# Performance work log

Hardware: AMD Instinct MI355X
Metric: run time of the kernel (lower is better)

Reference implementation:

```python
import jax, jax.numpy as jnp
import numpy as np

B, S, D_IN = 4, 2048, 1024
H, D_HEAD = 16, 64  # num_head, num_out; H*D_HEAD == D_IN here
LN_EPS = 1e-5


def setup_inputs() -> dict:
    key = jax.random.key(0)
    ks = jax.random.split(key, 5)
    scale = 1.0 / np.sqrt(D_IN)
    return {
        "x": jax.random.normal(ks[0], (B, S, D_IN), dtype=jnp.float32),
        "Wq": jax.random.normal(ks[1], (H * D_HEAD, D_IN), dtype=jnp.float32) * scale,
        "Wk": jax.random.normal(ks[2], (H * D_HEAD, D_IN), dtype=jnp.float32) * scale,
        "Wv": jax.random.normal(ks[3], (H * D_HEAD, D_IN), dtype=jnp.float32) * scale,
        "Wr": jax.random.normal(ks[4], (H * D_HEAD, D_IN), dtype=jnp.float32) * scale,
        "gamma": jnp.ones((H * D_HEAD,), dtype=jnp.float32),
        "beta": jnp.zeros((H * D_HEAD,), dtype=jnp.float32),
    }


def reference(x, Wq, Wk, Wv, Wr, gamma, beta):
    b, s, _ = x.shape
    # Linear (no bias), torch weight layout [out, in]; split heads head-major
    q = (x @ Wq.T).reshape(b, s, H, D_HEAD)
    k = (x @ Wk.T).reshape(b, s, H, D_HEAD)
    v = (x @ Wv.T).reshape(b, s, H, D_HEAD)
    # full O(S^2) score matrix, as in the original
    scores = jnp.einsum("bqhd,bkhd->bhqk", q, k) / jnp.sqrt(jnp.float32(D_HEAD))
    weights = jax.nn.softmax(scores, axis=-1)
    attn = jnp.einsum("bhqk,bkhd->bqhd", weights, v).reshape(b, s, H * D_HEAD)
    out = jax.nn.relu(attn + x @ Wr.T)
    # LayerNorm over last dim with affine params
    mu = jnp.mean(out, axis=-1, keepdims=True)
    var = jnp.mean(jnp.square(out - mu), axis=-1, keepdims=True)
    out = (out - mu) * jax.lax.rsqrt(var + LN_EPS) * gamma + beta
    return out
```

## Files before the change

kernel.cpp:

```cpp
#include <hip/hip_runtime.h>
#include <hip/hip_bf16.h>
#include <stdint.h>

constexpr int BB = 4;
constexpr int SS = 2048;
constexpr int DIN = 1024;
constexpr int HH = 16;
constexpr int DH = 64;
constexpr int NOUT = 4096;
constexpr int MROWS = BB * SS;

typedef __attribute__((ext_vector_type(8))) short bf16x8;
typedef __attribute__((ext_vector_type(8))) unsigned short u16x8;
typedef __attribute__((ext_vector_type(4))) unsigned short u16x4;
typedef __attribute__((ext_vector_type(4))) float f32x4;

__device__ __forceinline__ unsigned short f2bf(float f) {
  unsigned int x = __float_as_uint(f);
  unsigned int r = (x + 0x7fffu + ((x >> 16) & 1u)) >> 16;
  return (unsigned short)r;
}
__device__ __forceinline__ float bf2f(unsigned short u) {
  return __uint_as_float(((unsigned int)u) << 16);
}

__device__ __forceinline__ void gload16(const void* g, void* l) {
  typedef __attribute__((address_space(1))) void gvoid;
  typedef __attribute__((address_space(3))) void lvoid;
  __builtin_amdgcn_global_load_lds((gvoid*)(uintptr_t)g, (lvoid*)l, 16, 0, 0);
}

__global__ __launch_bounds__(256) void convert_x(const float* __restrict__ src,
                                                 unsigned short* __restrict__ dst) {
  int i = (blockIdx.x * 256 + threadIdx.x) * 8;
  f32x4 a = *(const f32x4*)(src + i);
  f32x4 b = *(const f32x4*)(src + i + 4);
  u16x8 o;
  o[0] = f2bf(a[0]); o[1] = f2bf(a[1]); o[2] = f2bf(a[2]); o[3] = f2bf(a[3]);
  o[4] = f2bf(b[0]); o[5] = f2bf(b[1]); o[6] = f2bf(b[2]); o[7] = f2bf(b[3]);
  *(u16x8*)(dst + i) = o;
}

__global__ __launch_bounds__(256) void convert_w(const float* __restrict__ Wq,
                                                 const float* __restrict__ Wk,
                                                 const float* __restrict__ Wv,
                                                 const float* __restrict__ Wr,
                                                 unsigned short* __restrict__ dst) {
  int i = (blockIdx.x * 256 + threadIdx.x) * 8;
  int seg = i >> 20;
  const float* src = (seg == 0) ? Wq : (seg == 1) ? Wk : (seg == 2) ? Wv : Wr;
  float scale = (seg == 0) ? 0.125f * 1.44269504088896f : 1.0f;
  int j = i & 1048575;
  f32x4 a = *(const f32x4*)(src + j);
  f32x4 b = *(const f32x4*)(src + j + 4);
  u16x8 o;
  o[0] = f2bf(a[0] * scale); o[1] = f2bf(a[1] * scale);
  o[2] = f2bf(a[2] * scale); o[3] = f2bf(a[3] * scale);
  o[4] = f2bf(b[0] * scale); o[5] = f2bf(b[1] * scale);
  o[6] = f2bf(b[2] * scale); o[7] = f2bf(b[3] * scale);
  *(u16x8*)(dst + i) = o;
}

constexpr int GBM = 128, GBN = 128, GBK = 64;

__global__ __launch_bounds__(256) void gemm_qkvr(const unsigned short* __restrict__ X,
                                                 const unsigned short* __restrict__ Wt,
                                                 unsigned short* __restrict__ Y) {
  const int K = DIN;
  const int nbn = NOUT / GBN;
  int bid = blockIdx.x;
  int idx = (bid & 7) * 256 + (bid >> 3);
  int bm = idx / nbn, bn = idx % nbn;
  int m0 = bm * GBM, n0 = bn * GBN;
  int t = threadIdx.x;
  int w = t >> 6, l = t & 63;
  int lg = l >> 4, ll = l & 15;
  int wm = (w >> 1) * 64, wn = (w & 1) * 64;

  __shared__ unsigned short As[2][GBM * GBK];
  __shared__ unsigned short Bs[2][GBN * GBK];

  f32x4 acc[4][4];
#pragma unroll
  for (int i = 0; i < 4; i++)
#pragma unroll
    for (int j = 0; j < 4; j++) acc[i][j] = (f32x4)0.0f;

  int grow = t >> 3;
  int gslot = t & 7;

  auto stage = [&](int kt, int bi) {
    int k0 = kt * GBK;
#pragma unroll
    for (int c = 0; c < 4; ++c) {
      int row = c * 32 + grow;
      int col = (gslot ^ (row & 7)) * 8;
      gload16(X + (size_t)(m0 + row) * K + k0 + col, &As[bi][c * 2048 + w * 512]);
      gload16(Wt + (size_t)(n0 + row) * K + k0 + col, &Bs[bi][c * 2048 + w * 512]);
    }
  };

  stage(0, 0);
  stage(1, 1);
  asm volatile("s_waitcnt vmcnt(8)" ::: "memory");
  __builtin_amdgcn_s_barrier();
  __builtin_amdgcn_sched_barrier(0);

  for (int kt = 0; kt < 16; ++kt) {
    int cur = kt & 1;
    bf16x8 af[4][2], bfr[4][2];
#pragma unroll
    for (int mt = 0; mt < 4; ++mt)
#pragma unroll
      for (int kk = 0; kk < 2; ++kk)
        af[mt][kk] = *(const bf16x8*)&As[cur][(wm + mt * 16 + ll) * GBK +
                                             ((kk * 4 + lg) ^ (ll & 7)) * 8];
#pragma unroll
    for (int nt = 0; nt < 4; ++nt)
#pragma unroll
      for (int kk = 0; kk < 2; ++kk)
        bfr[nt][kk] = *(const bf16x8*)&Bs[cur][(wn + nt * 16 + ll) * GBK +
                                              ((kk * 4 + lg) ^ (ll & 7)) * 8];
    asm volatile("s_waitcnt lgkmcnt(0)" ::: "memory");
    __builtin_amdgcn_s_barrier();
    __builtin_amdgcn_sched_barrier(0);

    stage((kt + 2) & 15, cur);

    __builtin_amdgcn_s_setprio(1);
#pragma unroll
    for (int mt = 0; mt < 4; ++mt)
#pragma unroll
      for (int nt = 0; nt < 4; ++nt)
#pragma unroll
        for (int kk = 0; kk < 2; ++kk)
          acc[mt][nt] = __builtin_amdgcn_mfma_f32_16x16x32_bf16(af[mt][kk], bfr[nt][kk],
                                                                acc[mt][nt], 0, 0, 0);
    __builtin_amdgcn_s_setprio(0);

    asm volatile("s_waitcnt vmcnt(8)" ::: "memory");
    __builtin_amdgcn_s_barrier();
    __builtin_amdgcn_sched_barrier(0);
  }
  asm volatile("s_waitcnt vmcnt(0)" ::: "memory");

#pragma unroll
  for (int mt = 0; mt < 4; ++mt)
#pragma unroll
    for (int nt = 0; nt < 4; ++nt) {
      int n = n0 + wn + nt * 16 + ll;
#pragma unroll
      for (int r = 0; r < 4; ++r) {
        int m = m0 + wm + mt * 16 + lg * 4 + r;
        Y[(size_t)m * NOUT + n] = f2bf(acc[mt][nt][r]);
      }
    }
}

__global__ __launch_bounds__(256) void transpose_v(const unsigned short* __restrict__ qkvr,
                                                   unsigned short* __restrict__ vt) {
  int bh = blockIdx.x >> 5;
  int st = blockIdx.x & 31;
  int b = bh >> 4, h = bh & 15;
  __shared__ unsigned short tile[64][72];
  int t = threadIdx.x;
#pragma unroll
  for (int c = 0; c < 2; ++c) {
    int chunk = t + c * 256;
    int row = chunk >> 3;
    int col = (chunk & 7) * 8;
    u16x8 v = *(const u16x8*)(qkvr + (size_t)(b * SS + st * 64 + row) * NOUT + 2048 + h * DH + col);
    *(u16x8*)&tile[row][col] = v;
  }
  __syncthreads();
  int d = t >> 2;
  int s0 = (t & 3) * 16;
  u16x8 o0, o1;
#pragma unroll
  for (int i = 0; i < 8; ++i) o0[i] = tile[s0 + i][d];
#pragma unroll
  for (int i = 0; i < 8; ++i) o1[i] = tile[s0 + 8 + i][d];
  size_t orow = (size_t)(bh * DH + d) * SS + st * 64 + s0;
  *(u16x8*)(vt + orow) = o0;
  *(u16x8*)(vt + orow + 8) = o1;
}

__global__ __launch_bounds__(512) void attention(const unsigned short* __restrict__ qkvr,
                                                 const unsigned short* __restrict__ vt,
                                                 unsigned short* __restrict__ attn) {
  int bid = blockIdx.x;
  int idx = (bid & 7) * 64 + (bid >> 3);
  int qt = idx & 7;
  int bh = idx >> 3;
  int b = bh >> 4, h = bh & 15;
  int t = threadIdx.x, w = t >> 6, l = t & 63;
  int lg = l >> 4, ll = l & 15;

  __shared__ unsigned short Ks[2][4096];
  __shared__ unsigned short Vs[2][4096];
  __shared__ unsigned short Ps[8][2048];

  const unsigned short* kbase = qkvr + (size_t)(b * SS) * NOUT + 1024 + h * DH;
  const unsigned short* vbase = vt + (size_t)(bh * DH) * SS;

  bf16x8 qb[2][2];
#pragma unroll
  for (int m = 0; m < 2; ++m) {
    int qrow = b * SS + qt * 256 + w * 32 + m * 16 + ll;
#pragma unroll
    for (int kk = 0; kk < 2; ++kk)
      qb[m][kk] = *(const bf16x8*)(qkvr + (size_t)qrow * NOUT + h * DH + kk * 32 + lg * 8);
  }

  f32x4 acc[2][4];
#pragma unroll
  for (int m = 0; m < 2; ++m)
#pragma unroll
    for (int i = 0; i < 4; i++) acc[m][i] = (f32x4)0.0f;
  float lsum[2] = {0.0f, 0.0f};

  int grow = t >> 3;
  int gcol = ((t & 7) ^ (grow & 7)) * 8;

  auto stage = [&](int tile, int bi) {
    gload16(kbase + (size_t)(tile * 64 + grow) * NOUT + gcol, &Ks[bi][w * 512]);
    gload16(vbase + (size_t)grow * SS + tile * 64 + gcol, &Vs[bi][w * 512]);
  };

  stage(0, 0);

  for (int kt = 0; kt < 32; ++kt) {
    int bi = kt & 1;
    stage((kt + 1) & 31, bi ^ 1);
    asm volatile("s_waitcnt vmcnt(2)" ::: "memory");
    __builtin_amdgcn_s_barrier();
    __builtin_amdgcn_sched_barrier(0);

    f32x4 s[2][4];
#pragma unroll
    for (int m = 0; m < 2; ++m)
#pragma unroll
      for (int nt = 0; nt < 4; nt++) s[m][nt] = (f32x4)0.0f;
    __builtin_amdgcn_s_setprio(1);
#pragma unroll
    for (int nt = 0; nt < 4; ++nt)
#pragma unroll
      for (int kk = 0; kk < 2; ++kk) {
        bf16x8 kb = *(const bf16x8*)&Ks[bi][(nt * 16 + ll) * 64 + ((kk * 4 + lg) ^ (ll & 7)) * 8];
        s[0][nt] = __builtin_amdgcn_mfma_f32_16x16x32_bf16(kb, qb[0][kk], s[0][nt], 0, 0, 0);
        s[1][nt] = __builtin_amdgcn_mfma_f32_16x16x32_bf16(kb, qb[1][kk], s[1][nt], 0, 0, 0);
      }
    __builtin_amdgcn_s_setprio(0);

#pragma unroll
    for (int m = 0; m < 2; ++m) {
      float ps = 0.0f;
#pragma unroll
      for (int nt = 0; nt < 4; nt++)
#pragma unroll
        for (int r = 0; r < 4; r++) {
          float e;
          asm("v_exp_f32 %0, %1" : "=v"(e) : "v"(s[m][nt][r]));
          s[m][nt][r] = e;
          ps += e;
        }
      lsum[m] += ps;
    }

#pragma unroll
    for (int m = 0; m < 2; ++m) {
      char* prow = (char*)&Ps[w][0] + (m * 16 + ll) * 128;
#pragma unroll
      for (int nt = 0; nt < 4; nt++) {
        unsigned sp0, sp1;
        asm("v_cvt_pk_bf16_f32 %0, %1, %2" : "=v"(sp0) : "v"(s[m][nt][0]), "v"(s[m][nt][1]));
        asm("v_cvt_pk_bf16_f32 %0, %1, %2" : "=v"(sp1) : "v"(s[m][nt][2]), "v"(s[m][nt][3]));
        uint2 pv; pv.x = sp0; pv.y = sp1;
        *(uint2*)(prow + ((2 * nt + (lg >> 1)) ^ (ll & 7)) * 16 + (lg & 1) * 8) = pv;
      }
    }

    bf16x8 pa[2][2];
#pragma unroll
    for (int m = 0; m < 2; ++m)
#pragma unroll
      for (int kk = 0; kk < 2; ++kk)
        pa[m][kk] = *(const bf16x8*)((char*)&Ps[w][0] + (m * 16 + ll) * 128 +
                                     ((4 * kk + lg) ^ (ll & 7)) * 16);

    __builtin_amdgcn_s_setprio(1);
#pragma unroll
    for (int kk = 0; kk < 2; ++kk) {
#pragma unroll
      for (int dt = 0; dt < 4; ++dt) {
        bf16x8 vb = *(const bf16x8*)&Vs[bi][(dt * 16 + ll) * 64 + ((kk * 4 + lg) ^ (ll & 7)) * 8];
        acc[0][dt] = __builtin_amdgcn_mfma_f32_16x16x32_bf16(pa[0][kk], vb, acc[0][dt], 0, 0, 0);
        acc[1][dt] = __builtin_amdgcn_mfma_f32_16x16x32_bf16(pa[1][kk], vb, acc[1][dt], 0, 0, 0);
      }
    }
    __builtin_amdgcn_s_setprio(0);
    __builtin_amdgcn_s_barrier();
    __builtin_amdgcn_sched_barrier(0);
  }
  asm volatile("s_waitcnt vmcnt(0)" ::: "memory");

  float inv[2][4];
#pragma unroll
  for (int m = 0; m < 2; ++m) {
    float lr = lsum[m];
    lr += __shfl_xor(lr, 16);
    lr += __shfl_xor(lr, 32);
#pragma unroll
    for (int r = 0; r < 4; r++)
      inv[m][r] = 1.0f / __shfl(lr, lg * 4 + r);
  }
#pragma unroll
  for (int m = 0; m < 2; ++m)
#pragma unroll
    for (int r = 0; r < 4; r++) {
      int arow = b * SS + qt * 256 + w * 32 + m * 16 + lg * 4 + r;
#pragma unroll
      for (int dt = 0; dt < 4; dt++)
        attn[(size_t)arow * DIN + h * DH + dt * 16 + ll] = f2bf(acc[m][dt][r] * inv[m][r]);
    }
}

__global__ __launch_bounds__(256) void ln_epilogue(const unsigned short* __restrict__ attn,
                                                   const unsigned short* __restrict__ qkvr,
                                                   const float* __restrict__ gamma,
                                                   const float* __restrict__ beta,
                                                   float* __restrict__ out) {
  int row = blockIdx.x;
  int t = threadIdx.x;
  u16x4 av = *(const u16x4*)(attn + (size_t)row * DIN + t * 4);
  u16x4 rv = *(const u16x4*)(qkvr + (size_t)row * NOUT + 3072 + t * 4);
  float v[4];
  float s = 0.0f, s2 = 0.0f;
#pragma unroll
  for (int i = 0; i < 4; i++) {
    v[i] = fmaxf(bf2f(av[i]) + bf2f(rv[i]), 0.0f);
    s += v[i];
    s2 += v[i] * v[i];
  }
#pragma unroll
  for (int m = 1; m < 64; m <<= 1) {
    s += __shfl_xor(s, m);
    s2 += __shfl_xor(s2, m);
  }
  __shared__ float red[2][4];
  int w = t >> 6, l = t & 63;
  if (l == 0) { red[0][w] = s; red[1][w] = s2; }
  __syncthreads();
  s = red[0][0] + red[0][1] + red[0][2] + red[0][3];
  s2 = red[1][0] + red[1][1] + red[1][2] + red[1][3];
  float mu = s * (1.0f / 1024.0f);
  float var = s2 * (1.0f / 1024.0f) - mu * mu;
  float rstd = rsqrtf(var + 1e-5f);
  f32x4 g = *(const f32x4*)(gamma + t * 4);
  f32x4 be = *(const f32x4*)(beta + t * 4);
  f32x4 o;
#pragma unroll
  for (int i = 0; i < 4; i++) o[i] = (v[i] - mu) * rstd * g[i] + be[i];
  *(f32x4*)(out + (size_t)row * DIN + t * 4) = o;
}

extern "C" void kernel_launch(void* const* d_in, const int* in_sizes, int n_in,
                              void* d_out, int out_size, void* d_ws, size_t ws_size,
                              hipStream_t stream) {
  const float* x = (const float*)d_in[0];
  const float* Wq = (const float*)d_in[1];
  const float* Wk = (const float*)d_in[2];
  const float* Wv = (const float*)d_in[3];
  const float* Wr = (const float*)d_in[4];
  const float* gamma = (const float*)d_in[5];
  const float* beta = (const float*)d_in[6];
  float* out = (float*)d_out;

  char* ws = (char*)d_ws;
  unsigned short* x_bf = (unsigned short*)ws;
  unsigned short* w_bf = (unsigned short*)(ws + (16ull << 20));
  unsigned short* qkvr = (unsigned short*)(ws + (24ull << 20));
  unsigned short* vt   = (unsigned short*)(ws + (88ull << 20));
  unsigned short* attn = (unsigned short*)(ws + (104ull << 20));

  convert_x<<<4096, 256, 0, stream>>>(x, x_bf);
  convert_w<<<2048, 256, 0, stream>>>(Wq, Wk, Wv, Wr, w_bf);
  gemm_qkvr<<<(MROWS / GBM) * (NOUT / GBN), 256, 0, stream>>>(x_bf, w_bf, qkvr);
  transpose_v<<<2048, 256, 0, stream>>>(qkvr, vt);
  attention<<<512, 512, 0, stream>>>(qkvr, vt, attn);
  ln_epilogue<<<MROWS, 256, 0, stream>>>(attn, qkvr, gamma, beta, out);
}
```

Before: 199.4 us.

## Reorder GEMM prefetch after MFMAs and compute softmax row sums with MFMA

In the projection GEMM, the LDS fragment loads are interleaved, and the wait, barrier and next-stage global prefetch now come after the MFMA block instead of before it. The sched_barriers are removed so the compiler can schedule more freely. In attention, the per-lane VALU accumulation of exp values is replaced by an extra MFMA against a ones vector that accumulates row sums, which also removes the final shuffle reduction. This moves VALU work onto the matrix units but sums the bf16-rounded probabilities rather than fp32 ones, and it reduces how much the GEMM prefetch overlaps with compute.

```diff
diff --git a/kernel.cpp b/kernel.cpp
--- a/kernel.cpp
+++ b/kernel.cpp
@@ -104,7 +104,6 @@
   stage(1, 1);
   asm volatile("s_waitcnt vmcnt(8)" ::: "memory");
   __builtin_amdgcn_s_barrier();
-  __builtin_amdgcn_sched_barrier(0);
 
   for (int kt = 0; kt < 16; ++kt) {
     int cur = kt & 1;
@@ -112,21 +111,12 @@
 #pragma unroll
     for (int mt = 0; mt < 4; ++mt)
 #pragma unroll
-      for (int kk = 0; kk < 2; ++kk)
+      for (int kk = 0; kk < 2; ++kk) {
         af[mt][kk] = *(const bf16x8*)&As[cur][(wm + mt * 16 + ll) * GBK +
                                              ((kk * 4 + lg) ^ (ll & 7)) * 8];
-#pragma unroll
-    for (int nt = 0; nt < 4; ++nt)
-#pragma unroll
-      for (int kk = 0; kk < 2; ++kk)
-        bfr[nt][kk] = *(const bf16x8*)&Bs[cur][(wn + nt * 16 + ll) * GBK +
+        bfr[mt][kk] = *(const bf16x8*)&Bs[cur][(wn + mt * 16 + ll) * GBK +
                                               ((kk * 4 + lg) ^ (ll & 7)) * 8];
-    asm volatile("s_waitcnt lgkmcnt(0)" ::: "memory");
-    __builtin_amdgcn_s_barrier();
-    __builtin_amdgcn_sched_barrier(0);
-
-    stage((kt + 2) & 15, cur);
-
+      }
     __builtin_amdgcn_s_setprio(1);
 #pragma unroll
     for (int mt = 0; mt < 4; ++mt)
@@ -138,9 +128,13 @@
                                                                 acc[mt][nt], 0, 0, 0);
     __builtin_amdgcn_s_setprio(0);
 
+    asm volatile("s_waitcnt lgkmcnt(0)" ::: "memory");
+    __builtin_amdgcn_s_barrier();
+
+    stage((kt + 2) & 15, cur);
+
     asm volatile("s_waitcnt vmcnt(8)" ::: "memory");
     __builtin_amdgcn_s_barrier();
-    __builtin_amdgcn_sched_barrier(0);
   }
   asm volatile("s_waitcnt vmcnt(0)" ::: "memory");
 
@@ -212,12 +206,18 @@
       qb[m][kk] = *(const bf16x8*)(qkvr + (size_t)qrow * NOUT + h * DH + kk * 32 + lg * 8);
   }
 
+  bf16x8 ones;
+#pragma unroll
+  for (int i = 0; i < 8; i++) ones[i] = (short)0x3F80;
+
   f32x4 acc[2][4];
-#pragma unroll
-  for (int m = 0; m < 2; ++m)
+  f32x4 dacc[2];
+#pragma unroll
+  for (int m = 0; m < 2; ++m) {
+    dacc[m] = (f32x4)0.0f;
 #pragma unroll
     for (int i = 0; i < 4; i++) acc[m][i] = (f32x4)0.0f;
-  float lsum[2] = {0.0f, 0.0f};
+  }
 
   int grow = t >> 3;
   int gcol = ((t & 7) ^ (grow & 7)) * 8;
@@ -253,8 +253,7 @@
     __builtin_amdgcn_s_setprio(0);
 
 #pragma unroll
-    for (int m = 0; m < 2; ++m) {
-      float ps = 0.0f;
+    for (int m = 0; m < 2; ++m)
 #pragma unroll
       for (int nt = 0; nt < 4; nt++)
 #pragma unroll
@@ -262,10 +261,7 @@
           float e;
           asm("v_exp_f32 %0, %1" : "=v"(e) : "v"(s[m][nt][r]));
           s[m][nt][r] = e;
-          ps += e;
         }
-      lsum[m] += ps;
-    }
 
 #pragma unroll
     for (int m = 0; m < 2; ++m) {
@@ -297,6 +293,8 @@
         acc[0][dt] = __builtin_amdgcn_mfma_f32_16x16x32_bf16(pa[0][kk], vb, acc[0][dt], 0, 0, 0);
         acc[1][dt] = __builtin_amdgcn_mfma_f32_16x16x32_bf16(pa[1][kk], vb, acc[1][dt], 0, 0, 0);
       }
+      dacc[0] = __builtin_amdgcn_mfma_f32_16x16x32_bf16(pa[0][kk], ones, dacc[0], 0, 0, 0);
+      dacc[1] = __builtin_amdgcn_mfma_f32_16x16x32_bf16(pa[1][kk], ones, dacc[1], 0, 0, 0);
     }
     __builtin_amdgcn_s_setprio(0);
     __builtin_amdgcn_s_barrier();
@@ -304,24 +302,15 @@
   }
   asm volatile("s_waitcnt vmcnt(0)" ::: "memory");
 
-  float inv[2][4];
-#pragma unroll
-  for (int m = 0; m < 2; ++m) {
-    float lr = lsum[m];
-    lr += __shfl_xor(lr, 16);
-    lr += __shfl_xor(lr, 32);
-#pragma unroll
-    for (int r = 0; r < 4; r++)
-      inv[m][r] = 1.0f / __shfl(lr, lg * 4 + r);
-  }
 #pragma unroll
   for (int m = 0; m < 2; ++m)
 #pragma unroll
     for (int r = 0; r < 4; r++) {
+      float inv = 1.0f / dacc[m][r];
       int arow = b * SS + qt * 256 + w * 32 + m * 16 + lg * 4 + r;
 #pragma unroll
       for (int dt = 0; dt < 4; dt++)
-        attn[(size_t)arow * DIN + h * DH + dt * 16 + ll] = f2bf(acc[m][dt][r] * inv[m][r]);
+        attn[(size_t)arow * DIN + h * DH + dt * 16 + ll] = f2bf(acc[m][dt][r] * inv);
     }
 }
 
```

Result: faster. 191.4 us (-4.0%).
